# Performance work log

Hardware: AMD Instinct MI355X
Metric: run time of the kernel (lower is better)

Reference implementation:

```python
import jax, jax.numpy as jnp
import numpy as np

B, C, H, W = 2, 64, 128, 240
DG = 8            # deformable groups
KH = KW = 3
K = KH * KW
PAD = 1
OFFSET_DIM = DG * 2 * K   # 144
MASK_DIM = DG * 1 * K     # 72


def conv2d(x, w, b):
    # x: [B,Cin,H,W], w: [Cout,Cin,kh,kw] -> [B,Cout,H,W], stride 1, pad 1
    y = jax.lax.conv_general_dilated(x, w, (1, 1), [(PAD, PAD), (PAD, PAD)],
                                     dimension_numbers=("NCHW", "OIHW", "NCHW"))
    return y + b[None, :, None, None]


def leaky_relu(x):
    return jnp.where(x >= 0, x, 0.1 * x)


def modulated_deform_conv(x, offset, mask, w, b):
    # x: [B,C,H,W]; offset: [B, DG*2*K, H, W]; mask: [B, DG*K, H, W] (already sigmoid-ed)
    # Convention: offset.reshape(B, DG, 2, K, H, W) -> [.. ,0,..]=dy, [..,1,..]=dx.
    Bx, Cx, Hx, Wx = x.shape
    cpg = Cx // DG
    ky = jnp.repeat(jnp.arange(KH) - PAD, KW).astype(x.dtype)   # [K]
    kx = jnp.tile(jnp.arange(KW) - PAD, KH).astype(x.dtype)     # [K]
    off = offset.reshape(Bx, DG, 2, K, Hx, Wx)
    hh = jnp.arange(Hx, dtype=x.dtype)
    ww = jnp.arange(Wx, dtype=x.dtype)
    py = off[:, :, 0] + hh[None, None, None, :, None] + ky[None, None, :, None, None]  # [B,DG,K,H,W]
    px = off[:, :, 1] + ww[None, None, None, None, :] + kx[None, None, :, None, None]
    y0 = jnp.floor(py)
    x0 = jnp.floor(px)
    wy = (py - y0).reshape(Bx, DG, 1, K, Hx * Wx)
    wx = (px - x0).reshape(Bx, DG, 1, K, Hx * Wx)
    y0i = y0.astype(jnp.int32)
    x0i = x0.astype(jnp.int32)
    xg = x.reshape(Bx, DG, cpg, Hx * Wx)

    def corner(yi, xi):
        valid = ((yi >= 0) & (yi < Hx) & (xi >= 0) & (xi < Wx)).astype(x.dtype)
        idx = (jnp.clip(yi, 0, Hx - 1) * Wx + jnp.clip(xi, 0, Wx - 1)).reshape(Bx, DG, K, Hx * Wx)
        gather = lambda xf, ix: xf[:, ix]                     # [cpg,K,HW]
        vals = jax.vmap(jax.vmap(gather))(xg, idx)            # [B,DG,cpg,K,HW]
        return vals * valid.reshape(Bx, DG, 1, K, Hx * Wx)

    v00 = corner(y0i, x0i)
    v01 = corner(y0i, x0i + 1)
    v10 = corner(y0i + 1, x0i)
    v11 = corner(y0i + 1, x0i + 1)
    sampled = (v00 * (1 - wy) * (1 - wx) + v01 * (1 - wy) * wx
               + v10 * wy * (1 - wx) + v11 * wy * wx)          # [B,DG,cpg,K,HW]
    sampled = sampled * mask.reshape(Bx, DG, 1, K, Hx * Wx)
    wr = w.reshape(w.shape[0], DG, cpg, K)
    out = jnp.einsum("ogck,bgckp->bop", wr, sampled).reshape(Bx, -1, Hx, Wx)
    return out + b[None, :, None, None]


def setup_inputs() -> dict:
    key = jax.random.key(0)
    ks = jax.random.split(key, 8)
    omd = OFFSET_DIM + MASK_DIM  # 216
    return {
        "nbr_fea": jax.random.normal(ks[0], (B, C, H, W), dtype=jnp.float32),
        "ref_fea": jax.random.normal(ks[1], (B, C, H, W), dtype=jnp.float32),
        # offset1_module_1: ConvReLU(2C -> C)
        "w1": 0.1 * jax.random.normal(ks[2], (C, 2 * C, 3, 3), dtype=jnp.float32),
        "b1": jnp.zeros((C,), dtype=jnp.float32),
        # offset1_module_2: Conv(C -> 216)
        "w2": 0.1 * jax.random.normal(ks[3], (omd, C, 3, 3), dtype=jnp.float32),
        "b2": jnp.zeros((omd,), dtype=jnp.float32),
        # modulated deform conv weight (C -> C)
        "wd": 0.1 * jax.random.normal(ks[4], (C, C, 3, 3), dtype=jnp.float32),
        "bd": jnp.zeros((C,), dtype=jnp.float32),
    }


def reference(nbr_fea, ref_fea, w1, b1, w2, b2, wd, bd):
    fea = jnp.concatenate([nbr_fea, ref_fea], axis=1)          # [B,2C,H,W]
    h = leaky_relu(conv2d(fea, w1, b1))                        # [B,C,H,W]
    offset_mask = conv2d(h, w2, b2)                            # [B,216,H,W]
    o1, o2, m = jnp.split(offset_mask, 3, axis=1)              # 72 each
    offset_curr = jnp.concatenate([o1, o2], axis=1)            # [B,144,H,W]
    mask = jax.nn.sigmoid(m)                                   # [B,72,H,W]
    aligned = modulated_deform_conv(nbr_fea, offset_curr, mask, wd, bd)
    return aligned, offset_curr
```

## Files before the change

kernel.cpp:

```cpp
#include <hip/hip_runtime.h>
#include <cstdint>
#include <cmath>

#define B_ 2
#define C_ 64
#define H_ 128
#define W_ 240
#define HW_ (H_*W_)
#define OFF_CH 144
#define MASK_CH 72
#define ALIGNED_SZ (B_*C_*HW_)

typedef __bf16 bf16x8 __attribute__((ext_vector_type(8)));
typedef float f32x4 __attribute__((ext_vector_type(4)));
typedef short short4v __attribute__((ext_vector_type(4)));
typedef unsigned short ushort_t;

__device__ __forceinline__ ushort_t f2bf(float f) {
    unsigned u = __float_as_uint(f);
    u += 0x7fffu + ((u >> 16) & 1u);
    return (ushort_t)(u >> 16);
}
__device__ __forceinline__ float bf2f(ushort_t b) {
    return __uint_as_float((unsigned)b << 16);
}
__device__ __forceinline__ float bf_lo(int q) {
    return __uint_as_float((unsigned)q << 16);
}
__device__ __forceinline__ float bf_hi(int q) {
    return __uint_as_float((unsigned)q & 0xffff0000u);
}

#define W1P_OFF  0u
#define W2P_OFF  147456u
#define PIN_OFF  442368u
#define HBUF_OFF 16171008u
#define MASK_OFF 24035328u
#define WDP_OFF  32882688u

__global__ __launch_bounds__(256) void pack_weights(
    const float* __restrict__ w1, const float* __restrict__ w2,
    const float* __restrict__ wd,
    ushort_t* __restrict__ w1pf, ushort_t* __restrict__ w2pf,
    ushort_t* __restrict__ wdp)
{
    int t = blockIdx.x * 256 + threadIdx.x;
    if (t < 73728) {
        int j = t & 7, lane = (t >> 3) & 63, r = t >> 9;
        int wv = r & 3, ct = r >> 2;
        int tap = ct % 9, chunk = ct / 9;
        int oc = wv * 16 + (lane & 15);
        int ci = chunk * 32 + ((lane >> 4) << 3) + j;
        w1pf[t] = f2bf(w1[((size_t)oc * 128 + ci) * 9 + tap]);
    } else if (t < 73728 + 147456) {
        int f = t - 73728;
        int j = f & 7, lane = (f >> 3) & 63, r = f >> 9;
        int wv = r & 3, q = r >> 2;
        int tap = q % 9, oc2 = q / 9;
        int chunk = oc2 & 1, ocg = oc2 >> 1;
        int oc = ocg * 64 + wv * 16 + (lane & 15);
        int ci = chunk * 32 + ((lane >> 4) << 3) + j;
        float v = (oc < 216) ? w2[((size_t)oc * 64 + ci) * 9 + tap] : 0.f;
        w2pf[f] = f2bf(v);
    } else if (t < 73728 + 147456 + 36864) {
        int f = t - 221184;
        int j = f & 7, lane = (f >> 3) & 63, sg = f >> 9;
        int g = sg & 3, s = sg >> 2;
        int oc = g * 16 + (lane & 15);
        int K = s * 32 + ((lane >> 4) << 3) + j;
        int dg = K / 72, rr = K - dg * 72;
        int tap = rr >> 3, ci = (dg << 3) + (rr & 7);
        wdp[f] = f2bf(wd[((size_t)oc * 64 + ci) * 9 + tap]);
    }
}

__global__ __launch_bounds__(256) void pack_input(
    const float* __restrict__ nbr, const float* __restrict__ ref,
    ushort_t* __restrict__ pin)
{
    int f = blockIdx.x * 256 + threadIdx.x;
    int civec = f & 15;
    int rem = f >> 4;
    int b = rem / HW_, pix = rem - b * HW_;
    const int half = civec >> 3;
    const float* src = (half == 0) ? (nbr + (size_t)b * 64 * HW_)
                                   : (ref + (size_t)b * 64 * HW_);
    int cbase = (civec & 7) * 8;
    union { ushort_t u[8]; int4 v; } o;
#pragma unroll
    for (int j = 0; j < 8; ++j)
        o.u[j] = f2bf(src[(size_t)(cbase + j) * HW_ + pix]);
    size_t dst;
    if (half == 0) {
        dst = (size_t)b * 2 * HW_ * 64 + (size_t)(civec & 7) * HW_ * 8 + (size_t)pix * 8;
    } else {
        dst = ((size_t)(b * 2 + 1) * HW_ + pix) * 64 + cbase;
    }
    *(int4*)&pin[dst] = o.v;
}

__global__ __launch_bounds__(256) void conv1_mfma(
    const ushort_t* __restrict__ pin, const float* __restrict__ b1,
    const ushort_t* __restrict__ w1pf, ushort_t* __restrict__ hbuf)
{
    const int bx = blockIdx.x, by = blockIdx.y, b = blockIdx.z;
    const int y0 = by << 1;
    const int x0 = bx * 48;
    const int tid = threadIdx.x;
    const int wv = tid >> 6, lane = tid & 63;
    const int l15 = lane & 15, k8 = (lane >> 4) << 3;

    __shared__ __align__(16) ushort_t s_in[4 * 50 * 40];

    f32x4 acc[2][3];
#pragma unroll
    for (int r = 0; r < 2; ++r)
#pragma unroll
        for (int i = 0; i < 3; ++i) acc[r][i] = (f32x4){0.f, 0.f, 0.f, 0.f};

    for (int chunk = 0; chunk < 4; ++chunk) {
        const int ci0 = chunk << 5;
        for (int i = tid; i < 800; i += 256) {
            int cvec = i & 3, rc = i >> 2;
            int row = rc / 50, col = rc - row * 50;
            int gy = y0 + row - 1, gx = x0 + col - 1;
            int ci = ci0 + cvec * 8;
            int half = ci >> 6, cw = ci & 63;
            int4 v = {0, 0, 0, 0};
            if ((unsigned)gy < (unsigned)H_ && (unsigned)gx < (unsigned)W_) {
                size_t srca;
                if (half == 0)
                    srca = (size_t)b * 2 * HW_ * 64 + (size_t)(cw >> 3) * HW_ * 8
                         + (size_t)(gy * W_ + gx) * 8;
                else
                    srca = ((size_t)(b * 2 + 1) * HW_ + (size_t)gy * W_ + gx) * 64 + cw;
                v = *(const int4*)&pin[srca];
            }
            *(int4*)&s_in[(row * 50 + col) * 40 + cvec * 8] = v;
        }
        bf16x8 af[9];
#pragma unroll
        for (int tap = 0; tap < 9; ++tap)
            af[tap] = *(const bf16x8*)&w1pf[((((size_t)chunk * 9 + tap) * 4 + wv) * 64 + lane) * 8];
        __syncthreads();

#pragma unroll
        for (int tap = 0; tap < 9; ++tap) {
            const int ky = tap / 3, kx = tap - ky * 3;
#pragma unroll
            for (int pt = 0; pt < 3; ++pt) {
                int col = (pt << 4) + l15 + kx;
#pragma unroll
                for (int r = 0; r < 2; ++r) {
                    bf16x8 bb = *(const bf16x8*)&s_in[(((r + ky) * 50) + col) * 40 + k8];
                    acc[r][pt] = __builtin_amdgcn_mfma_f32_16x16x32_bf16(af[tap], bb, acc[r][pt], 0, 0, 0);
                }
            }
        }
        __syncthreads();
    }

    const int ocb = (wv << 4) + ((lane >> 4) << 2);
    float bias[4];
#pragma unroll
    for (int r = 0; r < 4; ++r) bias[r] = b1[ocb + r];
#pragma unroll
    for (int r = 0; r < 2; ++r)
#pragma unroll
        for (int pt = 0; pt < 3; ++pt) {
            int gx = x0 + (pt << 4) + l15;
            union { ushort_t u[4]; short4v s; } o;
#pragma unroll
            for (int j = 0; j < 4; ++j) {
                float v = acc[r][pt][j] + bias[j];
                v = (v >= 0.f) ? v : 0.1f * v;
                o.u[j] = f2bf(v);
            }
            *(short4v*)&hbuf[(((size_t)b * H_ + y0 + r) * W_ + gx) * 64 + ocb] = o.s;
        }
}

__global__ __launch_bounds__(256) void conv2_mfma(
    const ushort_t* __restrict__ hbuf, const float* __restrict__ b2,
    const ushort_t* __restrict__ w2pf,
    float* __restrict__ off_out, ushort_t* __restrict__ maskbuf)
{
    const int bx = blockIdx.x, by = blockIdx.y;
    const int b = blockIdx.z >> 2, ocg = blockIdx.z & 3;
    const int y0 = by << 1;
    const int x0 = bx * 48;
    const int tid = threadIdx.x;
    const int wv = tid >> 6, lane = tid & 63;
    const int l15 = lane & 15, k8 = (lane >> 4) << 3;

    __shared__ __align__(16) ushort_t s_in[4 * 50 * 40];

    f32x4 acc[2][3];
#pragma unroll
    for (int r = 0; r < 2; ++r)
#pragma unroll
        for (int i = 0; i < 3; ++i) acc[r][i] = (f32x4){0.f, 0.f, 0.f, 0.f};

    for (int chunk = 0; chunk < 2; ++chunk) {
        const int ci0 = chunk << 5;
        for (int i = tid; i < 800; i += 256) {
            int cvec = i & 3, rc = i >> 2;
            int row = rc / 50, col = rc - row * 50;
            int gy = y0 + row - 1, gx = x0 + col - 1;
            int4 v = {0, 0, 0, 0};
            if ((unsigned)gy < (unsigned)H_ && (unsigned)gx < (unsigned)W_)
                v = *(const int4*)&hbuf[(((size_t)b * H_ + gy) * W_ + gx) * 64 + ci0 + cvec * 8];
            *(int4*)&s_in[(row * 50 + col) * 40 + cvec * 8] = v;
        }
        bf16x8 af[9];
#pragma unroll
        for (int tap = 0; tap < 9; ++tap)
            af[tap] = *(const bf16x8*)&w2pf[(((((size_t)ocg * 2 + chunk) * 9 + tap) * 4 + wv) * 64 + lane) * 8];
        __syncthreads();

#pragma unroll
        for (int tap = 0; tap < 9; ++tap) {
            const int ky = tap / 3, kx = tap - ky * 3;
#pragma unroll
            for (int pt = 0; pt < 3; ++pt) {
                int col = (pt << 4) + l15 + kx;
#pragma unroll
                for (int r = 0; r < 2; ++r) {
                    bf16x8 bb = *(const bf16x8*)&s_in[(((r + ky) * 50) + col) * 40 + k8];
                    acc[r][pt] = __builtin_amdgcn_mfma_f32_16x16x32_bf16(af[tap], bb, acc[r][pt], 0, 0, 0);
                }
            }
        }
        __syncthreads();
    }

    const int ocb = (wv << 4) + ((lane >> 4) << 2);
#pragma unroll
    for (int r = 0; r < 2; ++r)
#pragma unroll
        for (int pt = 0; pt < 3; ++pt) {
            int gx = x0 + (pt << 4) + l15;
#pragma unroll
            for (int j = 0; j < 4; ++j) {
                int co = (ocg << 6) + ocb + j;
                if (co < 216) {
                    float v = acc[r][pt][j] + b2[co];
                    if (co < 144) {
                        off_out[((size_t)b * OFF_CH + co) * HW_ + (size_t)(y0 + r) * W_ + gx] = v;
                    } else {
                        maskbuf[((size_t)b * MASK_CH + (co - 144)) * HW_ + (size_t)(y0 + r) * W_ + gx] =
                            f2bf(1.f / (1.f + expf(-v)));
                    }
                }
            }
        }
}

struct OffRec { float dy, dx, m; };
struct Stage  { int4 g0, g1, g2, g3; float w0, w1, w2, w3; };

__global__ __launch_bounds__(256, 4) void dconv_mfma(
    const ushort_t* __restrict__ pin,
    const float* __restrict__ offs,
    const ushort_t* __restrict__ maskbuf,
    const ushort_t* __restrict__ wdp, const float* __restrict__ bd,
    float* __restrict__ outp, ushort_t* __restrict__ partial)
{
    const int bid = blockIdx.x;
    const int kh  = (bid >= 960) ? 1 : 0;
    const int sb  = bid - kh * 960;
    const int nid = (sb & 7) * 120 + (sb >> 3);
    const int b   = nid / 480;
    const int rr_ = nid - b * 480;
    const int byt = rr_ / 15, bxt = rr_ - byt * 15;
    const int x0 = bxt << 4, y0 = byt << 2;
    const int base = kh * 9;

    const int tid = threadIdx.x;
    const int wv = tid >> 6, lane = tid & 63;
    const int l15 = lane & 15, hi4 = lane >> 4;

    const int x = x0 + l15, y = y0 + wv;
    const size_t pix = (size_t)y * W_ + x;
    const size_t pinb = (size_t)b * 2 * HW_ * 64;
    const float* offp = offs + (size_t)b * OFF_CH * HW_ + pix;
    const ushort_t* mkp = maskbuf + (size_t)b * MASK_CH * HW_ + pix;

    f32x4 acc0 = {0.f,0.f,0.f,0.f}, acc1 = {0.f,0.f,0.f,0.f};
    f32x4 acc2 = {0.f,0.f,0.f,0.f}, acc3 = {0.f,0.f,0.f,0.f};

    auto load_off = [&](int s) -> OffRec {
        int K = (s << 5) + (hi4 << 3);
        int dg = K / 72, r2 = K - dg * 72, tap = r2 >> 3;
        OffRec o;
        o.dy = offp[(size_t)(dg * 18 + tap) * HW_];
        o.dx = offp[(size_t)(dg * 18 + 9 + tap) * HW_];
        o.m  = bf2f(mkp[(size_t)(dg * 9 + tap) * HW_]);
        return o;
    };
    auto sample = [&](int s, OffRec of) -> Stage {
        int K = (s << 5) + (hi4 << 3);
        int dg = K / 72, rm = K - dg * 72, tap = rm >> 3;
        int ky = tap / 3 - 1, kx = tap % 3 - 1;
        float py  = (float)(y + ky) + of.dy;
        float pxf = (float)(x + kx) + of.dx;
        float yf = floorf(py), xf = floorf(pxf);
        float wy = py - yf, wx = pxf - xf;
        int yi = (int)yf, xi = (int)xf;
        bool y0v = (unsigned)yi < (unsigned)H_;
        bool y1v = (unsigned)(yi + 1) < (unsigned)H_;
        bool x0v = (unsigned)xi < (unsigned)W_;
        bool x1v = (unsigned)(xi + 1) < (unsigned)W_;
        Stage st;
        st.w0 = (y0v && x0v) ? (1.f - wy) * (1.f - wx) * of.m : 0.f;
        st.w1 = (y0v && x1v) ? (1.f - wy) * wx         * of.m : 0.f;
        st.w2 = (y1v && x0v) ? wy         * (1.f - wx) * of.m : 0.f;
        st.w3 = (y1v && x1v) ? wy         * wx         * of.m : 0.f;
        int yc0 = min(max(yi, 0), H_ - 1), yc1 = min(max(yi + 1, 0), H_ - 1);
        int xc0 = min(max(xi, 0), W_ - 1), xc1 = min(max(xi + 1, 0), W_ - 1);
        const size_t dgb = pinb + (size_t)dg * HW_ * 8;
        st.g0 = *(const int4*)&pin[dgb + (size_t)(yc0 * W_ + xc0) * 8];
        st.g1 = *(const int4*)&pin[dgb + (size_t)(yc0 * W_ + xc1) * 8];
        st.g2 = *(const int4*)&pin[dgb + (size_t)(yc1 * W_ + xc0) * 8];
        st.g3 = *(const int4*)&pin[dgb + (size_t)(yc1 * W_ + xc1) * 8];
        return st;
    };

    Stage  P0 = sample(base + 0, load_off(base + 0));
    Stage  P1 = sample(base + 1, load_off(base + 1));
    OffRec O0 = load_off(base + 2);
    OffRec O1 = load_off(base + 3);

#pragma unroll 2
    for (int ls = 0; ls < 9; ++ls) {
        const int s = base + ls;
        const ushort_t* wp = wdp + (((size_t)(s << 2) * 64) + lane) * 8;
        bf16x8 a0 = *(const bf16x8*)(wp);
        bf16x8 a1 = *(const bf16x8*)(wp + 512);
        bf16x8 a2 = *(const bf16x8*)(wp + 1024);
        bf16x8 a3 = *(const bf16x8*)(wp + 1536);

        Stage cur = (ls & 1) ? P1 : P0;
        bf16x8 bfrag;
        {
            const int* c00 = (const int*)&cur.g0; const int* c01 = (const int*)&cur.g1;
            const int* c10 = (const int*)&cur.g2; const int* c11 = (const int*)&cur.g3;
#pragma unroll
            for (int j = 0; j < 4; ++j) {
                float lo = cur.w0 * bf_lo(c00[j]) + cur.w1 * bf_lo(c01[j])
                         + cur.w2 * bf_lo(c10[j]) + cur.w3 * bf_lo(c11[j]);
                float hv = cur.w0 * bf_hi(c00[j]) + cur.w1 * bf_hi(c01[j])
                         + cur.w2 * bf_hi(c10[j]) + cur.w3 * bf_hi(c11[j]);
                bfrag[2 * j]     = (__bf16)lo;
                bfrag[2 * j + 1] = (__bf16)hv;
            }
        }

        int s2 = base + min(ls + 2, 8);
        if (ls & 1) P1 = sample(s2, O1); else P0 = sample(s2, O0);
        int s4 = base + min(ls + 4, 8);
        if (ls & 1) O1 = load_off(s4); else O0 = load_off(s4);

        acc0 = __builtin_amdgcn_mfma_f32_16x16x32_bf16(a0, bfrag, acc0, 0, 0, 0);
        acc1 = __builtin_amdgcn_mfma_f32_16x16x32_bf16(a1, bfrag, acc1, 0, 0, 0);
        acc2 = __builtin_amdgcn_mfma_f32_16x16x32_bf16(a2, bfrag, acc2, 0, 0, 0);
        acc3 = __builtin_amdgcn_mfma_f32_16x16x32_bf16(a3, bfrag, acc3, 0, 0, 0);
    }

    const int ocr = hi4 << 2;
    const size_t pbase = (size_t)b * C_ * HW_ + (size_t)y * W_ + x0 + l15;
    if (kh == 0) {
#pragma unroll
        for (int r = 0; r < 4; ++r) {
            int oc0 = ocr + r;
            outp[pbase + (size_t)(oc0)      * HW_] = acc0[r] + bd[oc0];
            outp[pbase + (size_t)(oc0 + 16) * HW_] = acc1[r] + bd[oc0 + 16];
            outp[pbase + (size_t)(oc0 + 32) * HW_] = acc2[r] + bd[oc0 + 32];
            outp[pbase + (size_t)(oc0 + 48) * HW_] = acc3[r] + bd[oc0 + 48];
        }
    } else {
#pragma unroll
        for (int r = 0; r < 4; ++r) {
            int oc0 = ocr + r;
            partial[pbase + (size_t)(oc0)      * HW_] = f2bf(acc0[r]);
            partial[pbase + (size_t)(oc0 + 16) * HW_] = f2bf(acc1[r]);
            partial[pbase + (size_t)(oc0 + 32) * HW_] = f2bf(acc2[r]);
            partial[pbase + (size_t)(oc0 + 48) * HW_] = f2bf(acc3[r]);
        }
    }
}

__global__ __launch_bounds__(256) void combine_half(
    float* __restrict__ outp, const ushort_t* __restrict__ part)
{
    size_t t = (size_t)(blockIdx.x * 256 + threadIdx.x) * 8;
    int4 p = *(const int4*)&part[t];
    const ushort_t* pu = (const ushort_t*)&p;
    float4 a = *(float4*)&outp[t];
    float4 c = *(float4*)&outp[t + 4];
    a.x += bf2f(pu[0]); a.y += bf2f(pu[1]); a.z += bf2f(pu[2]); a.w += bf2f(pu[3]);
    c.x += bf2f(pu[4]); c.y += bf2f(pu[5]); c.z += bf2f(pu[6]); c.w += bf2f(pu[7]);
    *(float4*)&outp[t] = a;
    *(float4*)&outp[t + 4] = c;
}

extern "C" void kernel_launch(void* const* d_in, const int* in_sizes, int n_in,
                              void* d_out, int out_size, void* d_ws, size_t ws_size,
                              hipStream_t stream)
{
    const float* nbr = (const float*)d_in[0];
    const float* ref = (const float*)d_in[1];
    const float* w1  = (const float*)d_in[2];
    const float* b1  = (const float*)d_in[3];
    const float* w2  = (const float*)d_in[4];
    const float* b2  = (const float*)d_in[5];
    const float* wd  = (const float*)d_in[6];
    const float* bd  = (const float*)d_in[7];

    float* out     = (float*)d_out;
    float* off_out = out + ALIGNED_SZ;

    char* ws = (char*)d_ws;
    ushort_t* w1pf  = (ushort_t*)(ws + W1P_OFF);
    ushort_t* w2pf  = (ushort_t*)(ws + W2P_OFF);
    ushort_t* pin   = (ushort_t*)(ws + PIN_OFF);
    ushort_t* hbufp = (ushort_t*)(ws + HBUF_OFF);
    ushort_t* maskp = (ushort_t*)(ws + MASK_OFF);
    ushort_t* wdp   = (ushort_t*)(ws + WDP_OFF);

    dim3 blk(256, 1, 1);
    pack_weights<<<1008, blk, 0, stream>>>(w1, w2, wd, w1pf, w2pf, wdp);
    pack_input<<<3840, blk, 0, stream>>>(nbr, ref, pin);
    conv1_mfma<<<dim3(5, 64, 2), blk, 0, stream>>>(pin, b1, w1pf, hbufp);
    conv2_mfma<<<dim3(5, 64, 8), blk, 0, stream>>>(hbufp, b2, w2pf, off_out, maskp);
    dconv_mfma<<<1920, blk, 0, stream>>>(pin, off_out, maskp, wdp, bd, out, hbufp);
    combine_half<<<1920, blk, 0, stream>>>(out, hbufp);
}
```

Before: 142.4 us.

## Use one output row per block and compute all conv2 channel groups per tile

conv1 now handles one output row per block instead of two, doubling the grid to 1280 blocks, which raises parallelism at the cost of loading a 3-row halo for every output row. conv2 also moves to one row per block, and each block now computes all four 64-channel output groups from a single shared-memory input tile instead of launching a separate block per group. This cuts the redundant reads of the hidden activations in conv2 by four, at the cost of 48 accumulator registers per thread and weight fragments being reloaded from global memory for each tap.

```diff
diff --git a/kernel.cpp b/kernel.cpp
--- a/kernel.cpp
+++ b/kernel.cpp
@@ -103,27 +103,24 @@
     const ushort_t* __restrict__ pin, const float* __restrict__ b1,
     const ushort_t* __restrict__ w1pf, ushort_t* __restrict__ hbuf)
 {
-    const int bx = blockIdx.x, by = blockIdx.y, b = blockIdx.z;
-    const int y0 = by << 1;
+    const int bx = blockIdx.x, y = blockIdx.y, b = blockIdx.z;
     const int x0 = bx * 48;
     const int tid = threadIdx.x;
     const int wv = tid >> 6, lane = tid & 63;
     const int l15 = lane & 15, k8 = (lane >> 4) << 3;
 
-    __shared__ __align__(16) ushort_t s_in[4 * 50 * 40];
-
-    f32x4 acc[2][3];
-#pragma unroll
-    for (int r = 0; r < 2; ++r)
-#pragma unroll
-        for (int i = 0; i < 3; ++i) acc[r][i] = (f32x4){0.f, 0.f, 0.f, 0.f};
+    __shared__ __align__(16) ushort_t s_in[3 * 50 * 40];
+
+    f32x4 acc[3];
+#pragma unroll
+    for (int i = 0; i < 3; ++i) acc[i] = (f32x4){0.f, 0.f, 0.f, 0.f};
 
     for (int chunk = 0; chunk < 4; ++chunk) {
         const int ci0 = chunk << 5;
-        for (int i = tid; i < 800; i += 256) {
+        for (int i = tid; i < 600; i += 256) {
             int cvec = i & 3, rc = i >> 2;
             int row = rc / 50, col = rc - row * 50;
-            int gy = y0 + row - 1, gx = x0 + col - 1;
+            int gy = y + row - 1, gx = x0 + col - 1;
             int ci = ci0 + cvec * 8;
             int half = ci >> 6, cw = ci & 63;
             int4 v = {0, 0, 0, 0};
@@ -150,11 +147,8 @@
 #pragma unroll
             for (int pt = 0; pt < 3; ++pt) {
                 int col = (pt << 4) + l15 + kx;
-#pragma unroll
-                for (int r = 0; r < 2; ++r) {
-                    bf16x8 bb = *(const bf16x8*)&s_in[(((r + ky) * 50) + col) * 40 + k8];
-                    acc[r][pt] = __builtin_amdgcn_mfma_f32_16x16x32_bf16(af[tap], bb, acc[r][pt], 0, 0, 0);
-                }
+                bf16x8 bb = *(const bf16x8*)&s_in[(ky * 50 + col) * 40 + k8];
+                acc[pt] = __builtin_amdgcn_mfma_f32_16x16x32_bf16(af[tap], bb, acc[pt], 0, 0, 0);
             }
         }
         __syncthreads();
@@ -165,19 +159,17 @@
 #pragma unroll
     for (int r = 0; r < 4; ++r) bias[r] = b1[ocb + r];
 #pragma unroll
-    for (int r = 0; r < 2; ++r)
-#pragma unroll
-        for (int pt = 0; pt < 3; ++pt) {
-            int gx = x0 + (pt << 4) + l15;
-            union { ushort_t u[4]; short4v s; } o;
-#pragma unroll
-            for (int j = 0; j < 4; ++j) {
-                float v = acc[r][pt][j] + bias[j];
-                v = (v >= 0.f) ? v : 0.1f * v;
-                o.u[j] = f2bf(v);
-            }
-            *(short4v*)&hbuf[(((size_t)b * H_ + y0 + r) * W_ + gx) * 64 + ocb] = o.s;
-        }
+    for (int pt = 0; pt < 3; ++pt) {
+        int gx = x0 + (pt << 4) + l15;
+        union { ushort_t u[4]; short4v s; } o;
+#pragma unroll
+        for (int r = 0; r < 4; ++r) {
+            float v = acc[pt][r] + bias[r];
+            v = (v >= 0.f) ? v : 0.1f * v;
+            o.u[r] = f2bf(v);
+        }
+        *(short4v*)&hbuf[(((size_t)b * H_ + y) * W_ + gx) * 64 + ocb] = o.s;
+    }
 }
 
 __global__ __launch_bounds__(256) void conv2_mfma(
@@ -185,50 +177,47 @@
     const ushort_t* __restrict__ w2pf,
     float* __restrict__ off_out, ushort_t* __restrict__ maskbuf)
 {
-    const int bx = blockIdx.x, by = blockIdx.y;
-    const int b = blockIdx.z >> 2, ocg = blockIdx.z & 3;
-    const int y0 = by << 1;
+    const int bx = blockIdx.x, y = blockIdx.y, b = blockIdx.z;
     const int x0 = bx * 48;
     const int tid = threadIdx.x;
     const int wv = tid >> 6, lane = tid & 63;
     const int l15 = lane & 15, k8 = (lane >> 4) << 3;
 
-    __shared__ __align__(16) ushort_t s_in[4 * 50 * 40];
-
-    f32x4 acc[2][3];
-#pragma unroll
-    for (int r = 0; r < 2; ++r)
-#pragma unroll
-        for (int i = 0; i < 3; ++i) acc[r][i] = (f32x4){0.f, 0.f, 0.f, 0.f};
+    __shared__ __align__(16) ushort_t s_in[3 * 50 * 40];
+
+    f32x4 acc[4][3];
+#pragma unroll
+    for (int g = 0; g < 4; ++g)
+#pragma unroll
+        for (int i = 0; i < 3; ++i) acc[g][i] = (f32x4){0.f, 0.f, 0.f, 0.f};
 
     for (int chunk = 0; chunk < 2; ++chunk) {
         const int ci0 = chunk << 5;
-        for (int i = tid; i < 800; i += 256) {
+        for (int i = tid; i < 600; i += 256) {
             int cvec = i & 3, rc = i >> 2;
             int row = rc / 50, col = rc - row * 50;
-            int gy = y0 + row - 1, gx = x0 + col - 1;
+            int gy = y + row - 1, gx = x0 + col - 1;
             int4 v = {0, 0, 0, 0};
             if ((unsigned)gy < (unsigned)H_ && (unsigned)gx < (unsigned)W_)
                 v = *(const int4*)&hbuf[(((size_t)b * H_ + gy) * W_ + gx) * 64 + ci0 + cvec * 8];
             *(int4*)&s_in[(row * 50 + col) * 40 + cvec * 8] = v;
         }
-        bf16x8 af[9];
-#pragma unroll
-        for (int tap = 0; tap < 9; ++tap)
-            af[tap] = *(const bf16x8*)&w2pf[(((((size_t)ocg * 2 + chunk) * 9 + tap) * 4 + wv) * 64 + lane) * 8];
         __syncthreads();
 
 #pragma unroll
         for (int tap = 0; tap < 9; ++tap) {
             const int ky = tap / 3, kx = tap - ky * 3;
+            bf16x8 af[4];
+#pragma unroll
+            for (int g = 0; g < 4; ++g)
+                af[g] = *(const bf16x8*)&w2pf[(((((size_t)g * 2 + chunk) * 9 + tap) * 4 + wv) * 64 + lane) * 8];
 #pragma unroll
             for (int pt = 0; pt < 3; ++pt) {
                 int col = (pt << 4) + l15 + kx;
-#pragma unroll
-                for (int r = 0; r < 2; ++r) {
-                    bf16x8 bb = *(const bf16x8*)&s_in[(((r + ky) * 50) + col) * 40 + k8];
-                    acc[r][pt] = __builtin_amdgcn_mfma_f32_16x16x32_bf16(af[tap], bb, acc[r][pt], 0, 0, 0);
-                }
+                bf16x8 bb = *(const bf16x8*)&s_in[(ky * 50 + col) * 40 + k8];
+#pragma unroll
+                for (int g = 0; g < 4; ++g)
+                    acc[g][pt] = __builtin_amdgcn_mfma_f32_16x16x32_bf16(af[g], bb, acc[g][pt], 0, 0, 0);
             }
         }
         __syncthreads();
@@ -236,19 +225,19 @@
 
     const int ocb = (wv << 4) + ((lane >> 4) << 2);
 #pragma unroll
-    for (int r = 0; r < 2; ++r)
+    for (int g = 0; g < 4; ++g)
 #pragma unroll
         for (int pt = 0; pt < 3; ++pt) {
             int gx = x0 + (pt << 4) + l15;
 #pragma unroll
-            for (int j = 0; j < 4; ++j) {
-                int co = (ocg << 6) + ocb + j;
+            for (int r = 0; r < 4; ++r) {
+                int co = (g << 6) + ocb + r;
                 if (co < 216) {
-                    float v = acc[r][pt][j] + b2[co];
+                    float v = acc[g][pt][r] + b2[co];
                     if (co < 144) {
-                        off_out[((size_t)b * OFF_CH + co) * HW_ + (size_t)(y0 + r) * W_ + gx] = v;
+                        off_out[((size_t)b * OFF_CH + co) * HW_ + y * W_ + gx] = v;
                     } else {
-                        maskbuf[((size_t)b * MASK_CH + (co - 144)) * HW_ + (size_t)(y0 + r) * W_ + gx] =
+                        maskbuf[((size_t)b * MASK_CH + (co - 144)) * HW_ + y * W_ + gx] =
                             f2bf(1.f / (1.f + expf(-v)));
                     }
                 }
@@ -431,8 +420,8 @@
     dim3 blk(256, 1, 1);
     pack_weights<<<1008, blk, 0, stream>>>(w1, w2, wd, w1pf, w2pf, wdp);
     pack_input<<<3840, blk, 0, stream>>>(nbr, ref, pin);
-    conv1_mfma<<<dim3(5, 64, 2), blk, 0, stream>>>(pin, b1, w1pf, hbufp);
-    conv2_mfma<<<dim3(5, 64, 8), blk, 0, stream>>>(hbufp, b2, w2pf, off_out, maskp);
+    conv1_mfma<<<dim3(5, 128, 2), blk, 0, stream>>>(pin, b1, w1pf, hbufp);
+    conv2_mfma<<<dim3(5, 128, 2), blk, 0, stream>>>(hbufp, b2, w2pf, off_out, maskp);
     dconv_mfma<<<1920, blk, 0, stream>>>(pin, off_out, maskp, wdp, bd, out, hbufp);
     combine_half<<<1920, blk, 0, stream>>>(out, hbufp);
 }
```

Measured after the change: 146.7 us. 3.0% more time.
